# Kernel optimization log

Measured on AMD Instinct MI355X. Metric: run time of the kernel, lower is better.

The kernel has to match this reference:

```python
import jax, jax.numpy as jnp
import numpy as np

B, T, D = 64, 1024, 512
H, O = 512, 128
HALF = D // 2
ALPHA_M = 0.8


def setup_inputs() -> dict:
    key = jax.random.key(0)
    ks = jax.random.split(key, 6)
    s_in = 1.0 / np.sqrt(HALF)
    s_h = 1.0 / np.sqrt(H)
    return {
        "x": jax.random.normal(ks[0], (B, T, D), dtype=jnp.float32),
        "w1": jax.random.uniform(ks[1], (H, HALF), jnp.float32, -s_in, s_in),
        "b1": jnp.zeros((H,), jnp.float32),
        "tau1": jnp.full((H,), 3.0, jnp.float32),
        "w2": jax.random.uniform(ks[2], (H, HALF), jnp.float32, -s_in, s_in),
        "b2": jnp.zeros((H,), jnp.float32),
        "tau2": jnp.full((H,), 0.5, jnp.float32),
        "wo": jax.random.uniform(ks[3], (O, H), jnp.float32, -s_h, s_h),
        "bo": jnp.zeros((O,), jnp.float32),
    }


def reference(x, w1, b1, tau1, w2, b2, tau2, wo, bo):
    # Hoist the per-timestep branch Linears into two batched GEMMs.
    d1_in = jnp.einsum("bti,hi->tbh", x[:, :, :HALF], w1) + b1  # [T,B,H]
    d2_in = jnp.einsum("bti,hi->tbh", x[:, :, HALF:], w2) + b2  # [T,B,H]

    a1 = jax.nn.sigmoid(tau1)  # [H]
    a2 = jax.nn.sigmoid(tau2)  # [H]

    def step(carry, ins):
        d1, d2, mem = carry
        i1, i2 = ins
        d1 = a1 * d1 + (1.0 - a1) * i1
        d2 = a2 * d2 + (1.0 - a2) * i2
        mem = ALPHA_M * mem + (1.0 - ALPHA_M) * (d1 + d2)
        return (d1, d2, mem), mem

    z = jnp.zeros((x.shape[0], tau1.shape[0]), x.dtype)
    _, mems = jax.lax.scan(step, (z, z, z), (d1_in, d2_in))  # mems: [T,B,H]

    # Output projection + sigmoid, vectorized over all timesteps.
    out = jax.nn.sigmoid(jnp.einsum("tbh,oh->bto", mems, wo) + bo)  # [B,T,O]
    return out
```

## Files before the change

kernel.cpp:

```cpp
#include <hip/hip_runtime.h>


#define B_    64
#define T_    1024
#define D_    512
#define H_    512
#define O_    128
#define HALF_ 256
#define CLEN  32
#define NC    32

typedef __attribute__((ext_vector_type(4))) float        f32x4;
typedef __attribute__((ext_vector_type(2))) float        f32x2;
typedef __attribute__((ext_vector_type(8))) short        s16x8;
typedef __attribute__((ext_vector_type(4))) unsigned int u32x4;

__device__ __forceinline__ unsigned short f2bf(float f) {
    unsigned u = __float_as_uint(f);
    return (unsigned short)((u + 0x7fffu + ((u >> 16) & 1u)) >> 16);
}
__device__ __forceinline__ unsigned packbf(float a, float b) {
    return (unsigned)f2bf(a) | ((unsigned)f2bf(b) << 16);
}
__device__ __forceinline__ float bflo(unsigned u) { return __uint_as_float(u << 16); }
__device__ __forceinline__ float bfhi(unsigned u) { return __uint_as_float(u & 0xffff0000u); }
__device__ __forceinline__ float sigf(float x) { return 1.f / (1.f + __expf(-x)); }
__device__ __forceinline__ float guard(float dn) {
    if (fabsf(dn) < 1e-6f) dn = (dn < 0.f ? -1e-6f : 1e-6f);
    return dn;
}
__device__ __forceinline__ float pw32(float a) {
    float t = a * a; t *= t; t *= t; t *= t; t *= t; return t;
}

typedef const __attribute__((address_space(1))) unsigned int gu32;
typedef __attribute__((address_space(3))) unsigned int      lu32;
__device__ __forceinline__ void gl_lds16(const void* g, void* l) {
    __builtin_amdgcn_global_load_lds((gu32*)g, (lu32*)l, 16, 0, 0);
}

__global__ __launch_bounds__(256) void gtab_kernel(
    const float* __restrict__ tau1, const float* __restrict__ tau2,
    float* __restrict__ G1, float* __restrict__ G2)
{
    const int h = blockIdx.x * 256 + threadIdx.x;
    const float a1 = sigf(tau1[h]), a2 = sigf(tau2[h]);
    const float c1 = 0.2f * a1 / guard(0.8f - a1);
    const float c2 = 0.2f * a2 / guard(0.8f - a2);
    float pm = 1.f, p1 = 1.f, p2 = 1.f;
    for (int k = 0; k < CLEN; ++k) {
        pm *= 0.8f; p1 *= a1; p2 *= a2;
        G1[k * H_ + h] = c1 * (pm - p1);
        G2[k * H_ + h] = c2 * (pm - p2);
    }
}

__global__ __launch_bounds__(256) void cast_kernel(const float* __restrict__ x,
                                                   unsigned int* __restrict__ xb) {
    size_t i = ((size_t)blockIdx.x * 256 + threadIdx.x) * 8;
    f32x4 a = *(const f32x4*)(x + i);
    f32x4 b = *(const f32x4*)(x + i + 4);
    u32x4 p;
    p.x = packbf(a.x, a.y); p.y = packbf(a.z, a.w);
    p.z = packbf(b.x, b.y); p.w = packbf(b.z, b.w);
    *(u32x4*)(xb + i / 2) = p;
}

__global__ __launch_bounds__(256, 2) void gemm1f_kernel(
    const unsigned short* __restrict__ xb, const float* __restrict__ w1,
    const float* __restrict__ w2,
    const float* __restrict__ b1, const float* __restrict__ tau1,
    const float* __restrict__ b2, const float* __restrict__ tau2,
    unsigned int* __restrict__ mems,
    float* __restrict__ Sd1, float* __restrict__ Sd2, float* __restrict__ Sm)
{
    __shared__ short smem[32768];
    short* As  = smem;
    short* Bs  = smem + 8192;
    short* d1L = smem + 16384;
    short* d2L = smem;

    const int nt = blockIdx.x;
    const int mt = blockIdx.y;
    const int b  = mt >> 3;
    const int t0 = (mt & 7) << 7;

    const int tid = threadIdx.x, l = tid & 63, wv = tid >> 6;
    const int ln = l & 15, qd = l >> 4;
    const int wm = (wv & 1) << 6, wn = (wv >> 1) << 6;

    for (int br = 0; br < 2; ++br) {
        const float* w = br ? w2 : w1;
        const unsigned short* abase = xb + (size_t)(mt * 128) * D_ + br * HALF_;
        const float* wbase = w + (size_t)(nt * 128) * HALF_;

        f32x4 acc[4][4] = {};

        for (int kt = 0; kt < HALF_; kt += 64) {
            #pragma unroll
            for (int i = 0; i < 4; ++i) {
                int ch = wv * 4 + i;
                int r  = ch * 8 + (l >> 3);
                int kbl = (l & 7) ^ (r & 7);
                gl_lds16(abase + (size_t)r * D_ + kt + kbl * 8, &As[ch * 512 + l * 8]);
            }
            #pragma unroll
            for (int i = 0; i < 4; ++i) {
                int gi = i * 256 + tid;
                int r = gi >> 3, kbp = gi & 7, kbl = kbp ^ (r & 7);
                const float* src = wbase + (size_t)r * HALF_ + kt + kbl * 8;
                f32x4 b0 = *(const f32x4*)src;
                f32x4 b1v = *(const f32x4*)(src + 4);
                u32x4 pb;
                pb.x = packbf(b0.x, b0.y); pb.y = packbf(b0.z, b0.w);
                pb.z = packbf(b1v.x, b1v.y); pb.w = packbf(b1v.z, b1v.w);
                *(u32x4*)&Bs[r * 64 + kbp * 8] = pb;
            }
            __syncthreads();
            #pragma unroll
            for (int ks = 0; ks < 64; ks += 32) {
                s16x8 af[4], bfv[4];
                #pragma unroll
                for (int i = 0; i < 4; ++i) {
                    int r = wm + i * 16 + ln;
                    int kbp = ((ks >> 3) + qd) ^ (r & 7);
                    af[i] = *(const s16x8*)&As[r * 64 + kbp * 8];
                }
                #pragma unroll
                for (int j = 0; j < 4; ++j) {
                    int r = wn + j * 16 + ln;
                    int kbp = ((ks >> 3) + qd) ^ (r & 7);
                    bfv[j] = *(const s16x8*)&Bs[r * 64 + kbp * 8];
                }
                #pragma unroll
                for (int i = 0; i < 4; ++i)
                    #pragma unroll
                    for (int j = 0; j < 4; ++j)
                        acc[i][j] = __builtin_amdgcn_mfma_f32_16x16x32_bf16(
                            af[i], bfv[j], acc[i][j], 0, 0, 0);
            }
            __syncthreads();
        }

        short* dL = br ? d2L : d1L;
        #pragma unroll
        for (int i = 0; i < 4; ++i)
            #pragma unroll
            for (int j = 0; j < 4; ++j)
                #pragma unroll
                for (int r = 0; r < 4; ++r)
                    dL[(wm + i * 16 + qd * 4 + r) * 128 + wn + j * 16 + ln] =
                        (short)f2bf(acc[i][j][r]);
    }
    __syncthreads();

    const int cl  = tid >> 6;
    const int h2l = tid & 63;
    const int hl0 = h2l << 1;
    const int hg0 = nt * 128 + hl0;
    const int cg  = ((mt & 7) << 2) + cl;

    const float a1a = sigf(tau1[hg0]), a1b = sigf(tau1[hg0 + 1]);
    const float a2a = sigf(tau2[hg0]), a2b = sigf(tau2[hg0 + 1]);
    const float o1a = 1.f - a1a, o1b = 1.f - a1b;
    const float o2a = 1.f - a2a, o2b = 1.f - a2b;
    const float bb1a = b1[hg0], bb1b = b1[hg0 + 1];
    const float bb2a = b2[hg0], bb2b = b2[hg0 + 1];

    float d1a = 0.f, d1b = 0.f, d2a = 0.f, d2b = 0.f, ma = 0.f, mb = 0.f;
    const size_t mrow = (size_t)(b * T_ + t0 + cl * CLEN) * (H_ / 2) + nt * 64 + h2l;

    #pragma unroll 8
    for (int k = 0; k < CLEN; ++k) {
        unsigned u1 = *(const unsigned*)&d1L[(cl * CLEN + k) * 128 + hl0];
        unsigned u2 = *(const unsigned*)&d2L[(cl * CLEN + k) * 128 + hl0];
        float i1a = bflo(u1) + bb1a, i1b = bfhi(u1) + bb1b;
        float i2a = bflo(u2) + bb2a, i2b = bfhi(u2) + bb2b;
        d1a = a1a * d1a + o1a * i1a;  d1b = a1b * d1b + o1b * i1b;
        d2a = a2a * d2a + o2a * i2a;  d2b = a2b * d2b + o2b * i2b;
        ma = 0.8f * ma + 0.2f * (d1a + d2a);
        mb = 0.8f * mb + 0.2f * (d1b + d2b);
        mems[mrow + (size_t)k * (H_ / 2)] = packbf(ma, mb);
    }

    const size_t si = (size_t)(cg * B_ + b) * H_ + hg0;
    f32x2 v;
    v.x = d1a; v.y = d1b; *(f32x2*)&Sd1[si] = v;
    v.x = d2a; v.y = d2b; *(f32x2*)&Sd2[si] = v;
    v.x = ma;  v.y = mb;  *(f32x2*)&Sm[si]  = v;
}

__global__ __launch_bounds__(128) void scanB_kernel(
    const float* __restrict__ Sd1, const float* __restrict__ Sd2,
    const float* __restrict__ Sm,
    const float* __restrict__ tau1, const float* __restrict__ tau2,
    float* __restrict__ D1, float* __restrict__ D2, float* __restrict__ DM)
{
    const int g = blockIdx.x * 128 + threadIdx.x;
    const int h2 = g & 255, b = g >> 8, h0 = h2 << 1;

    const float a1a = sigf(tau1[h0]), a1b = sigf(tau1[h0 + 1]);
    const float a2a = sigf(tau2[h0]), a2b = sigf(tau2[h0 + 1]);
    const float amL = pw32(0.8f);
    const float a1La = pw32(a1a), a1Lb = pw32(a1b);
    const float a2La = pw32(a2a), a2Lb = pw32(a2b);

    const float c1a = 0.2f * a1a / guard(0.8f - a1a);
    const float c1b = 0.2f * a1b / guard(0.8f - a1b);
    const float c2a = 0.2f * a2a / guard(0.8f - a2a);
    const float c2b = 0.2f * a2b / guard(0.8f - a2b);

    const float g1La = c1a * (amL - a1La), g1Lb = c1b * (amL - a1Lb);
    const float g2La = c2a * (amL - a2La), g2Lb = c2b * (amL - a2Lb);

    float D1a = 0.f, D1b = 0.f, D2a = 0.f, D2b = 0.f, Ma = 0.f, Mb = 0.f;
    for (int c = 0; c < NC; ++c) {
        const size_t si = (size_t)(c * B_ + b) * H_ + h0;
        f32x2 v;
        v.x = D1a; v.y = D1b; *(f32x2*)&D1[si] = v;
        v.x = D2a; v.y = D2b; *(f32x2*)&D2[si] = v;
        v.x = Ma;  v.y = Mb;  *(f32x2*)&DM[si] = v;
        f32x2 s1 = *(const f32x2*)&Sd1[si];
        f32x2 s2 = *(const f32x2*)&Sd2[si];
        f32x2 sm = *(const f32x2*)&Sm[si];
        float nMa = amL * Ma + D1a * g1La + D2a * g2La + sm.x;
        float nMb = amL * Mb + D1b * g1Lb + D2b * g2Lb + sm.y;
        D1a = a1La * D1a + s1.x;  D1b = a1Lb * D1b + s1.y;
        D2a = a2La * D2a + s2.x;  D2b = a2Lb * D2b + s2.y;
        Ma = nMa;  Mb = nMb;
    }
}

__global__ __launch_bounds__(256, 2) void gemm2f_kernel(
    const unsigned short* __restrict__ mems, const float* __restrict__ wo,
    const float* __restrict__ bo,
    const float* __restrict__ G1, const float* __restrict__ G2,
    const float* __restrict__ D1, const float* __restrict__ D2,
    const float* __restrict__ DM, float* __restrict__ out)
{
    __shared__ short As[128 * 64];
    __shared__ short Bs[128 * 64];
    __shared__ float PMl[CLEN];

    const int mt = blockIdx.x;
    const int b = mt >> 3, c0 = (mt & 7) << 2;
    const int tid = threadIdx.x, l = tid & 63, wv = tid >> 6;
    const int ln = l & 15, qd = l >> 4;
    const int wm = (wv & 1) << 6, wn = (wv >> 1) << 6;

    if (tid < CLEN) {
        float pm = 1.f;
        for (int k = 0; k <= tid; ++k) pm *= 0.8f;
        PMl[tid] = pm;
    }
    __syncthreads();

    f32x4 acc[4][4] = {};
    const unsigned short* abase = mems + (size_t)(mt * 128) * H_;

    for (int kt = 0; kt < H_; kt += 64) {
        #pragma unroll
        for (int i = 0; i < 4; ++i) {
            int gi = i * 256 + tid;
            int r = gi >> 3, kbp = gi & 7, kbl = kbp ^ (r & 7);
            int h0 = kt + kbl * 8;
            int k = r & 31, c = c0 + (r >> 5);
            size_t dbase = (size_t)(c * B_ + b) * H_ + h0;
            f32x4 d1a = *(const f32x4*)&D1[dbase], d1b = *(const f32x4*)&D1[dbase + 4];
            f32x4 d2a = *(const f32x4*)&D2[dbase], d2b = *(const f32x4*)&D2[dbase + 4];
            f32x4 dma = *(const f32x4*)&DM[dbase], dmb = *(const f32x4*)&DM[dbase + 4];
            f32x4 g1a = *(const f32x4*)&G1[k * H_ + h0], g1b = *(const f32x4*)&G1[k * H_ + h0 + 4];
            f32x4 g2a = *(const f32x4*)&G2[k * H_ + h0], g2b = *(const f32x4*)&G2[k * H_ + h0 + 4];
            float pm = PMl[k];
            u32x4 mv = *(const u32x4*)(abase + (size_t)r * H_ + h0);
            float v0 = bflo(mv.x) + d1a.x * g1a.x + d2a.x * g2a.x + dma.x * pm;
            float v1 = bfhi(mv.x) + d1a.y * g1a.y + d2a.y * g2a.y + dma.y * pm;
            float v2 = bflo(mv.y) + d1a.z * g1a.z + d2a.z * g2a.z + dma.z * pm;
            float v3 = bfhi(mv.y) + d1a.w * g1a.w + d2a.w * g2a.w + dma.w * pm;
            float v4 = bflo(mv.z) + d1b.x * g1b.x + d2b.x * g2b.x + dmb.x * pm;
            float v5 = bfhi(mv.z) + d1b.y * g1b.y + d2b.y * g2b.y + dmb.y * pm;
            float v6 = bflo(mv.w) + d1b.z * g1b.z + d2b.z * g2b.z + dmb.z * pm;
            float v7 = bfhi(mv.w) + d1b.w * g1b.w + d2b.w * g2b.w + dmb.w * pm;
            u32x4 p;
            p.x = packbf(v0, v1); p.y = packbf(v2, v3);
            p.z = packbf(v4, v5); p.w = packbf(v6, v7);
            *(u32x4*)&As[r * 64 + kbp * 8] = p;
        }
        #pragma unroll
        for (int i = 0; i < 4; ++i) {
            int gi = i * 256 + tid;
            int r = gi >> 3, kbp = gi & 7, kbl = kbp ^ (r & 7);
            const float* src = wo + (size_t)r * H_ + kt + kbl * 8;
            f32x4 b0 = *(const f32x4*)src;
            f32x4 b1v = *(const f32x4*)(src + 4);
            u32x4 pb;
            pb.x = packbf(b0.x, b0.y); pb.y = packbf(b0.z, b0.w);
            pb.z = packbf(b1v.x, b1v.y); pb.w = packbf(b1v.z, b1v.w);
            *(u32x4*)&Bs[r * 64 + kbp * 8] = pb;
        }
        __syncthreads();
        #pragma unroll
        for (int ks = 0; ks < 64; ks += 32) {
            s16x8 af[4], bfv[4];
            #pragma unroll
            for (int i = 0; i < 4; ++i) {
                int r = wm + i * 16 + ln;
                int kbp = ((ks >> 3) + qd) ^ (r & 7);
                af[i] = *(const s16x8*)&As[r * 64 + kbp * 8];
            }
            #pragma unroll
            for (int j = 0; j < 4; ++j) {
                int r = wn + j * 16 + ln;
                int kbp = ((ks >> 3) + qd) ^ (r & 7);
                bfv[j] = *(const s16x8*)&Bs[r * 64 + kbp * 8];
            }
            #pragma unroll
            for (int i = 0; i < 4; ++i)
                #pragma unroll
                for (int j = 0; j < 4; ++j)
                    acc[i][j] = __builtin_amdgcn_mfma_f32_16x16x32_bf16(
                        af[i], bfv[j], acc[i][j], 0, 0, 0);
        }
        __syncthreads();
    }

    float bov[4];
    #pragma unroll
    for (int j = 0; j < 4; ++j) bov[j] = bo[wn + j * 16 + ln];

    float* orow = out + (size_t)(mt * 128 + wm + qd * 4) * O_ + wn + ln;
    #pragma unroll
    for (int i = 0; i < 4; ++i)
        #pragma unroll
        for (int j = 0; j < 4; ++j)
            #pragma unroll
            for (int r = 0; r < 4; ++r) {
                float v = acc[i][j][r] + bov[j];
                orow[(size_t)(i * 16 + r) * O_ + j * 16] = 1.f / (1.f + __expf(-v));
            }
}

extern "C" void kernel_launch(void* const* d_in, const int* in_sizes, int n_in,
                              void* d_out, int out_size, void* d_ws, size_t ws_size,
                              hipStream_t stream) {
    const float* x    = (const float*)d_in[0];
    const float* w1   = (const float*)d_in[1];
    const float* b1   = (const float*)d_in[2];
    const float* tau1 = (const float*)d_in[3];
    const float* w2   = (const float*)d_in[4];
    const float* b2   = (const float*)d_in[5];
    const float* tau2 = (const float*)d_in[6];
    const float* wo   = (const float*)d_in[7];
    const float* bo   = (const float*)d_in[8];
    float* out = (float*)d_out;

    char* w = (char*)d_ws;
    unsigned short* xb   = (unsigned short*)(w);
    unsigned int*   mems = (unsigned int*)(w + (size_t)64 * 1024 * 1024);
    float* Sd1 = (float*)(w + (size_t)128 * 1024 * 1024);
    float* Sd2 = Sd1 + (1u << 20);
    float* Sm  = Sd1 + (2u << 20);
    float* D1  = Sd1 + (3u << 20);
    float* D2  = Sd1 + (4u << 20);
    float* DM  = Sd1 + (5u << 20);
    float* G1  = Sd1 + (6u << 20);
    float* G2  = G1 + CLEN * H_;

    gtab_kernel<<<dim3(2), 256, 0, stream>>>(tau1, tau2, G1, G2);
    cast_kernel<<<dim3(16384), 256, 0, stream>>>(x, (unsigned int*)xb);
    gemm1f_kernel<<<dim3(4, 512), 256, 0, stream>>>(xb, w1, w2, b1, tau1, b2, tau2,
                                                    mems, Sd1, Sd2, Sm);
    scanB_kernel<<<dim3(128), 128, 0, stream>>>(Sd1, Sd2, Sm, tau1, tau2, D1, D2, DM);
    gemm2f_kernel<<<dim3(512), 256, 0, stream>>>((const unsigned short*)mems, wo, bo,
                                                 G1, G2, D1, D2, DM, out);
}
```

Baseline: 364.8 us.

## Fuse x bf16 cast into gemm1, precast weights, halve scan chunk length

Removes the separate cast of x to bf16, which wrote and reread a 64 MB intermediate. gemm1 now reads fp32 x directly and converts it to bf16 while staging. The weights are precast once to bf16 by a small kernel so the GEMMs can load them asynchronously straight into LDS. gemm1 is restructured so each block owns 64 rows and loops over all four H tiles, so x is read once per block; it uses smaller tiles and targets higher occupancy. The chunk length drops to 16, giving 64 chunks, which shortens the serial scan per chunk but doubles the carry state that scanB has to combine.

```diff
diff --git a/kernel.cpp b/kernel.cpp
--- a/kernel.cpp
+++ b/kernel.cpp
@@ -7,8 +7,8 @@
 #define H_    512
 #define O_    128
 #define HALF_ 256
-#define CLEN  32
-#define NC    32
+#define CLEN  16
+#define NC    64
 
 typedef __attribute__((ext_vector_type(4))) float        f32x4;
 typedef __attribute__((ext_vector_type(2))) float        f32x2;
@@ -29,14 +29,32 @@
     if (fabsf(dn) < 1e-6f) dn = (dn < 0.f ? -1e-6f : 1e-6f);
     return dn;
 }
-__device__ __forceinline__ float pw32(float a) {
-    float t = a * a; t *= t; t *= t; t *= t; t *= t; return t;
+__device__ __forceinline__ float pw16(float a) {
+    float t = a * a; t *= t; t *= t; t *= t; return t;
 }
 
 typedef const __attribute__((address_space(1))) unsigned int gu32;
 typedef __attribute__((address_space(3))) unsigned int      lu32;
 __device__ __forceinline__ void gl_lds16(const void* g, void* l) {
     __builtin_amdgcn_global_load_lds((gu32*)g, (lu32*)l, 16, 0, 0);
+}
+
+__global__ __launch_bounds__(256) void wcast_kernel(
+    const float* __restrict__ w1, const float* __restrict__ w2,
+    const float* __restrict__ wo, unsigned int* __restrict__ dst)
+{
+    int g = blockIdx.x * 256 + threadIdx.x;
+    int i = g * 8;
+    const float* src; int off;
+    if (i < 131072)      { src = w1; off = i; }
+    else if (i < 262144) { src = w2; off = i - 131072; }
+    else                 { src = wo; off = i - 262144; }
+    f32x4 a = *(const f32x4*)(src + off);
+    f32x4 b = *(const f32x4*)(src + off + 4);
+    u32x4 p;
+    p.x = packbf(a.x, a.y); p.y = packbf(a.z, a.w);
+    p.z = packbf(b.x, b.y); p.w = packbf(b.z, b.w);
+    *(u32x4*)(dst + i / 2) = p;
 }
 
 __global__ __launch_bounds__(256) void gtab_kernel(
@@ -55,139 +73,138 @@
     }
 }
 
-__global__ __launch_bounds__(256) void cast_kernel(const float* __restrict__ x,
-                                                   unsigned int* __restrict__ xb) {
-    size_t i = ((size_t)blockIdx.x * 256 + threadIdx.x) * 8;
-    f32x4 a = *(const f32x4*)(x + i);
-    f32x4 b = *(const f32x4*)(x + i + 4);
-    u32x4 p;
-    p.x = packbf(a.x, a.y); p.y = packbf(a.z, a.w);
-    p.z = packbf(b.x, b.y); p.w = packbf(b.z, b.w);
-    *(u32x4*)(xb + i / 2) = p;
-}
-
-__global__ __launch_bounds__(256, 2) void gemm1f_kernel(
-    const unsigned short* __restrict__ xb, const float* __restrict__ w1,
-    const float* __restrict__ w2,
+__global__ __launch_bounds__(256, 4) void gemm1f_kernel(
+    const float* __restrict__ x,
+    const unsigned short* __restrict__ w1b, const unsigned short* __restrict__ w2b,
     const float* __restrict__ b1, const float* __restrict__ tau1,
     const float* __restrict__ b2, const float* __restrict__ tau2,
     unsigned int* __restrict__ mems,
     float* __restrict__ Sd1, float* __restrict__ Sd2, float* __restrict__ Sm)
 {
-    __shared__ short smem[32768];
-    short* As  = smem;
-    short* Bs  = smem + 8192;
-    short* d1L = smem + 16384;
-    short* d2L = smem;
-
-    const int nt = blockIdx.x;
-    const int mt = blockIdx.y;
-    const int b  = mt >> 3;
-    const int t0 = (mt & 7) << 7;
+    __shared__ short smem[20480];
+    short* As = smem;
+    short* Bs = smem + 4096;
+
+    const int mt = blockIdx.x;
+    const int b  = mt >> 4;
+    const int tb = mt & 15;
+    const int m0 = mt * 64;
 
     const int tid = threadIdx.x, l = tid & 63, wv = tid >> 6;
     const int ln = l & 15, qd = l >> 4;
-    const int wm = (wv & 1) << 6, wn = (wv >> 1) << 6;
-
-    for (int br = 0; br < 2; ++br) {
-        const float* w = br ? w2 : w1;
-        const unsigned short* abase = xb + (size_t)(mt * 128) * D_ + br * HALF_;
-        const float* wbase = w + (size_t)(nt * 128) * HALF_;
-
-        f32x4 acc[4][4] = {};
-
-        for (int kt = 0; kt < HALF_; kt += 64) {
-            #pragma unroll
-            for (int i = 0; i < 4; ++i) {
-                int ch = wv * 4 + i;
-                int r  = ch * 8 + (l >> 3);
-                int kbl = (l & 7) ^ (r & 7);
-                gl_lds16(abase + (size_t)r * D_ + kt + kbl * 8, &As[ch * 512 + l * 8]);
+    const int wm = (wv & 1) << 5;
+    const int wn = (wv >> 1) << 6;
+
+    for (int nt = 0; nt < 4; ++nt) {
+        for (int br = 0; br < 2; ++br) {
+            const unsigned short* wbase = (br ? w2b : w1b) + (size_t)(nt * 128) * HALF_;
+            const float* ab = x + (size_t)m0 * D_ + br * HALF_;
+
+            f32x4 acc[2][4] = {};
+
+            for (int kt = 0; kt < HALF_; kt += 64) {
+                #pragma unroll
+                for (int i = 0; i < 4; ++i) {
+                    int ch = wv * 4 + i;
+                    int r  = ch * 8 + (l >> 3);
+                    int kbl = (l & 7) ^ (r & 7);
+                    gl_lds16(wbase + (size_t)r * HALF_ + kt + kbl * 8,
+                             &Bs[ch * 512 + l * 8]);
+                }
+                #pragma unroll
+                for (int i = 0; i < 2; ++i) {
+                    int gi = i * 256 + tid;
+                    int r = gi >> 3, kbp = gi & 7, kbl = kbp ^ (r & 7);
+                    const float* src = ab + (size_t)r * D_ + kt + kbl * 8;
+                    f32x4 a0 = *(const f32x4*)src;
+                    f32x4 a1v = *(const f32x4*)(src + 4);
+                    u32x4 pa;
+                    pa.x = packbf(a0.x, a0.y); pa.y = packbf(a0.z, a0.w);
+                    pa.z = packbf(a1v.x, a1v.y); pa.w = packbf(a1v.z, a1v.w);
+                    *(u32x4*)&As[r * 64 + kbp * 8] = pa;
+                }
+                __syncthreads();
+                #pragma unroll
+                for (int ks = 0; ks < 64; ks += 32) {
+                    s16x8 af[2], bfv[4];
+                    #pragma unroll
+                    for (int i = 0; i < 2; ++i) {
+                        int r = wm + i * 16 + ln;
+                        int kbp = ((ks >> 3) + qd) ^ (r & 7);
+                        af[i] = *(const s16x8*)&As[r * 64 + kbp * 8];
+                    }
+                    #pragma unroll
+                    for (int j = 0; j < 4; ++j) {
+                        int r = wn + j * 16 + ln;
+                        int kbp = ((ks >> 3) + qd) ^ (r & 7);
+                        bfv[j] = *(const s16x8*)&Bs[r * 64 + kbp * 8];
+                    }
+                    #pragma unroll
+                    for (int i = 0; i < 2; ++i)
+                        #pragma unroll
+                        for (int j = 0; j < 4; ++j)
+                            acc[i][j] = __builtin_amdgcn_mfma_f32_16x16x32_bf16(
+                                af[i], bfv[j], acc[i][j], 0, 0, 0);
+                }
+                __syncthreads();
             }
-            #pragma unroll
-            for (int i = 0; i < 4; ++i) {
-                int gi = i * 256 + tid;
-                int r = gi >> 3, kbp = gi & 7, kbl = kbp ^ (r & 7);
-                const float* src = wbase + (size_t)r * HALF_ + kt + kbl * 8;
-                f32x4 b0 = *(const f32x4*)src;
-                f32x4 b1v = *(const f32x4*)(src + 4);
-                u32x4 pb;
-                pb.x = packbf(b0.x, b0.y); pb.y = packbf(b0.z, b0.w);
-                pb.z = packbf(b1v.x, b1v.y); pb.w = packbf(b1v.z, b1v.w);
-                *(u32x4*)&Bs[r * 64 + kbp * 8] = pb;
-            }
-            __syncthreads();
-            #pragma unroll
-            for (int ks = 0; ks < 64; ks += 32) {
-                s16x8 af[4], bfv[4];
-                #pragma unroll
-                for (int i = 0; i < 4; ++i) {
-                    int r = wm + i * 16 + ln;
-                    int kbp = ((ks >> 3) + qd) ^ (r & 7);
-                    af[i] = *(const s16x8*)&As[r * 64 + kbp * 8];
-                }
-                #pragma unroll
-                for (int j = 0; j < 4; ++j) {
-                    int r = wn + j * 16 + ln;
-                    int kbp = ((ks >> 3) + qd) ^ (r & 7);
-                    bfv[j] = *(const s16x8*)&Bs[r * 64 + kbp * 8];
-                }
-                #pragma unroll
-                for (int i = 0; i < 4; ++i)
+
+            short* dS = br ? smem : (smem + 12288);
+            #pragma unroll
+            for (int i = 0; i < 2; ++i)
+                #pragma unroll
+                for (int j = 0; j < 4; ++j)
                     #pragma unroll
-                    for (int j = 0; j < 4; ++j)
-                        acc[i][j] = __builtin_amdgcn_mfma_f32_16x16x32_bf16(
-                            af[i], bfv[j], acc[i][j], 0, 0, 0);
-            }
-            __syncthreads();
-        }
-
-        short* dL = br ? d2L : d1L;
-        #pragma unroll
-        for (int i = 0; i < 4; ++i)
-            #pragma unroll
-            for (int j = 0; j < 4; ++j)
-                #pragma unroll
-                for (int r = 0; r < 4; ++r)
-                    dL[(wm + i * 16 + qd * 4 + r) * 128 + wn + j * 16 + ln] =
-                        (short)f2bf(acc[i][j][r]);
-    }
-    __syncthreads();
-
-    const int cl  = tid >> 6;
-    const int h2l = tid & 63;
-    const int hl0 = h2l << 1;
-    const int hg0 = nt * 128 + hl0;
-    const int cg  = ((mt & 7) << 2) + cl;
-
-    const float a1a = sigf(tau1[hg0]), a1b = sigf(tau1[hg0 + 1]);
-    const float a2a = sigf(tau2[hg0]), a2b = sigf(tau2[hg0 + 1]);
-    const float o1a = 1.f - a1a, o1b = 1.f - a1b;
-    const float o2a = 1.f - a2a, o2b = 1.f - a2b;
-    const float bb1a = b1[hg0], bb1b = b1[hg0 + 1];
-    const float bb2a = b2[hg0], bb2b = b2[hg0 + 1];
-
-    float d1a = 0.f, d1b = 0.f, d2a = 0.f, d2b = 0.f, ma = 0.f, mb = 0.f;
-    const size_t mrow = (size_t)(b * T_ + t0 + cl * CLEN) * (H_ / 2) + nt * 64 + h2l;
-
-    #pragma unroll 8
-    for (int k = 0; k < CLEN; ++k) {
-        unsigned u1 = *(const unsigned*)&d1L[(cl * CLEN + k) * 128 + hl0];
-        unsigned u2 = *(const unsigned*)&d2L[(cl * CLEN + k) * 128 + hl0];
-        float i1a = bflo(u1) + bb1a, i1b = bfhi(u1) + bb1b;
-        float i2a = bflo(u2) + bb2a, i2b = bfhi(u2) + bb2b;
-        d1a = a1a * d1a + o1a * i1a;  d1b = a1b * d1b + o1b * i1b;
-        d2a = a2a * d2a + o2a * i2a;  d2b = a2b * d2b + o2b * i2b;
-        ma = 0.8f * ma + 0.2f * (d1a + d2a);
-        mb = 0.8f * mb + 0.2f * (d1b + d2b);
-        mems[mrow + (size_t)k * (H_ / 2)] = packbf(ma, mb);
-    }
-
-    const size_t si = (size_t)(cg * B_ + b) * H_ + hg0;
-    f32x2 v;
-    v.x = d1a; v.y = d1b; *(f32x2*)&Sd1[si] = v;
-    v.x = d2a; v.y = d2b; *(f32x2*)&Sd2[si] = v;
-    v.x = ma;  v.y = mb;  *(f32x2*)&Sm[si]  = v;
+                    for (int r = 0; r < 4; ++r) {
+                        int t = wm + i * 16 + qd * 4 + r;
+                        int h = wn + j * 16 + ln;
+                        int word = t * 64 + ((h >> 1) ^ (qd << 3));
+                        dS[word * 2 + (h & 1)] = (short)f2bf(acc[i][j][r]);
+                    }
+        }
+        __syncthreads();
+
+        const int cl  = tid >> 6;
+        const int h2l = tid & 63;
+        const int hg0 = nt * 128 + (h2l << 1);
+        const int cg  = tb * 4 + cl;
+
+        const float a1a = sigf(tau1[hg0]), a1b = sigf(tau1[hg0 + 1]);
+        const float a2a = sigf(tau2[hg0]), a2b = sigf(tau2[hg0 + 1]);
+        const float o1a = 1.f - a1a, o1b = 1.f - a1b;
+        const float o2a = 1.f - a2a, o2b = 1.f - a2b;
+        const float bb1a = b1[hg0], bb1b = b1[hg0 + 1];
+        const float bb2a = b2[hg0], bb2b = b2[hg0 + 1];
+
+        const unsigned* d1p = (const unsigned*)(smem + 12288);
+        const unsigned* d2p = (const unsigned*)smem;
+
+        float d1a = 0.f, d1b = 0.f, d2a = 0.f, d2b = 0.f, ma = 0.f, mb = 0.f;
+        const size_t mrow = ((size_t)(b * T_ + tb * 64 + cl * CLEN)) * (H_ / 2)
+                            + nt * 64 + h2l;
+
+        #pragma unroll
+        for (int k = 0; k < CLEN; ++k) {
+            int tw = (cl * CLEN + k) * 64;
+            int sw = h2l ^ (((k >> 2) & 3) << 3);
+            unsigned u1 = d1p[tw + sw];
+            unsigned u2 = d2p[tw + sw];
+            float i1a = bflo(u1) + bb1a, i1b = bfhi(u1) + bb1b;
+            float i2a = bflo(u2) + bb2a, i2b = bfhi(u2) + bb2b;
+            d1a = a1a * d1a + o1a * i1a;  d1b = a1b * d1b + o1b * i1b;
+            d2a = a2a * d2a + o2a * i2a;  d2b = a2b * d2b + o2b * i2b;
+            ma = 0.8f * ma + 0.2f * (d1a + d2a);
+            mb = 0.8f * mb + 0.2f * (d1b + d2b);
+            mems[mrow + (size_t)k * (H_ / 2)] = packbf(ma, mb);
+        }
+
+        const size_t si = (size_t)(cg * B_ + b) * H_ + hg0;
+        f32x2 v;
+        v.x = d1a; v.y = d1b; *(f32x2*)&Sd1[si] = v;
+        v.x = d2a; v.y = d2b; *(f32x2*)&Sd2[si] = v;
+        v.x = ma;  v.y = mb;  *(f32x2*)&Sm[si]  = v;
+        __syncthreads();
+    }
 }
 
 __global__ __launch_bounds__(128) void scanB_kernel(
@@ -201,9 +218,9 @@
 
     const float a1a = sigf(tau1[h0]), a1b = sigf(tau1[h0 + 1]);
     const float a2a = sigf(tau2[h0]), a2b = sigf(tau2[h0 + 1]);
-    const float amL = pw32(0.8f);
-    const float a1La = pw32(a1a), a1Lb = pw32(a1b);
-    const float a2La = pw32(a2a), a2Lb = pw32(a2b);
+    const float amL = pw16(0.8f);
+    const float a1La = pw16(a1a), a1Lb = pw16(a1b);
+    const float a2La = pw16(a2a), a2Lb = pw16(a2b);
 
     const float c1a = 0.2f * a1a / guard(0.8f - a1a);
     const float c1b = 0.2f * a1b / guard(0.8f - a1b);
@@ -232,7 +249,7 @@
 }
 
 __global__ __launch_bounds__(256, 2) void gemm2f_kernel(
-    const unsigned short* __restrict__ mems, const float* __restrict__ wo,
+    const unsigned short* __restrict__ mems, const unsigned short* __restrict__ wob,
     const float* __restrict__ bo,
     const float* __restrict__ G1, const float* __restrict__ G2,
     const float* __restrict__ D1, const float* __restrict__ D2,
@@ -243,7 +260,7 @@
     __shared__ float PMl[CLEN];
 
     const int mt = blockIdx.x;
-    const int b = mt >> 3, c0 = (mt & 7) << 2;
+    const int b = mt >> 3, c0 = (mt & 7) << 3;
     const int tid = threadIdx.x, l = tid & 63, wv = tid >> 6;
     const int ln = l & 15, qd = l >> 4;
     const int wm = (wv & 1) << 6, wn = (wv >> 1) << 6;
@@ -261,10 +278,17 @@
     for (int kt = 0; kt < H_; kt += 64) {
         #pragma unroll
         for (int i = 0; i < 4; ++i) {
+            int ch = wv * 4 + i;
+            int r  = ch * 8 + (l >> 3);
+            int kbl = (l & 7) ^ (r & 7);
+            gl_lds16(wob + (size_t)r * H_ + kt + kbl * 8, &Bs[ch * 512 + l * 8]);
+        }
+        #pragma unroll
+        for (int i = 0; i < 4; ++i) {
             int gi = i * 256 + tid;
             int r = gi >> 3, kbp = gi & 7, kbl = kbp ^ (r & 7);
             int h0 = kt + kbl * 8;
-            int k = r & 31, c = c0 + (r >> 5);
+            int k = r & (CLEN - 1), c = c0 + (r >> 4);
             size_t dbase = (size_t)(c * B_ + b) * H_ + h0;
             f32x4 d1a = *(const f32x4*)&D1[dbase], d1b = *(const f32x4*)&D1[dbase + 4];
             f32x4 d2a = *(const f32x4*)&D2[dbase], d2b = *(const f32x4*)&D2[dbase + 4];
@@ -286,18 +310,6 @@
             p.z = packbf(v4, v5); p.w = packbf(v6, v7);
             *(u32x4*)&As[r * 64 + kbp * 8] = p;
         }
-        #pragma unroll
-        for (int i = 0; i < 4; ++i) {
-            int gi = i * 256 + tid;
-            int r = gi >> 3, kbp = gi & 7, kbl = kbp ^ (r & 7);
-            const float* src = wo + (size_t)r * H_ + kt + kbl * 8;
-            f32x4 b0 = *(const f32x4*)src;
-            f32x4 b1v = *(const f32x4*)(src + 4);
-            u32x4 pb;
-            pb.x = packbf(b0.x, b0.y); pb.y = packbf(b0.z, b0.w);
-            pb.z = packbf(b1v.x, b1v.y); pb.w = packbf(b1v.z, b1v.w);
-            *(u32x4*)&Bs[r * 64 + kbp * 8] = pb;
-        }
         __syncthreads();
         #pragma unroll
         for (int ks = 0; ks < 64; ks += 32) {
@@ -354,23 +366,26 @@
     const float* bo   = (const float*)d_in[8];
     float* out = (float*)d_out;
 
-    char* w = (char*)d_ws;
-    unsigned short* xb   = (unsigned short*)(w);
-    unsigned int*   mems = (unsigned int*)(w + (size_t)64 * 1024 * 1024);
-    float* Sd1 = (float*)(w + (size_t)128 * 1024 * 1024);
-    float* Sd2 = Sd1 + (1u << 20);
-    float* Sm  = Sd1 + (2u << 20);
-    float* D1  = Sd1 + (3u << 20);
-    float* D2  = Sd1 + (4u << 20);
-    float* DM  = Sd1 + (5u << 20);
-    float* G1  = Sd1 + (6u << 20);
+    char* wsp = (char*)d_ws;
+    unsigned int* mems = (unsigned int*)wsp;
+    float* Sd1 = (float*)(wsp + (size_t)64 * 1024 * 1024);
+    const size_t SARR = (size_t)NC * B_ * H_;
+    float* Sd2 = Sd1 + SARR;
+    float* Sm  = Sd1 + 2 * SARR;
+    float* D1  = Sd1 + 3 * SARR;
+    float* D2  = Sd1 + 4 * SARR;
+    float* DM  = Sd1 + 5 * SARR;
+    float* G1  = Sd1 + 6 * SARR;
     float* G2  = G1 + CLEN * H_;
-
+    unsigned short* w1b = (unsigned short*)(G2 + CLEN * H_);
+    unsigned short* w2b = w1b + 131072;
+    unsigned short* wob = w2b + 131072;
+
+    wcast_kernel<<<dim3(160), 256, 0, stream>>>(w1, w2, wo, (unsigned int*)w1b);
     gtab_kernel<<<dim3(2), 256, 0, stream>>>(tau1, tau2, G1, G2);
-    cast_kernel<<<dim3(16384), 256, 0, stream>>>(x, (unsigned int*)xb);
-    gemm1f_kernel<<<dim3(4, 512), 256, 0, stream>>>(xb, w1, w2, b1, tau1, b2, tau2,
-                                                    mems, Sd1, Sd2, Sm);
+    gemm1f_kernel<<<dim3(1024), 256, 0, stream>>>(x, w1b, w2b, b1, tau1, b2, tau2,
+                                                  mems, Sd1, Sd2, Sm);
     scanB_kernel<<<dim3(128), 128, 0, stream>>>(Sd1, Sd2, Sm, tau1, tau2, D1, D2, DM);
-    gemm2f_kernel<<<dim3(512), 256, 0, stream>>>((const unsigned short*)mems, wo, bo,
+    gemm2f_kernel<<<dim3(512), 256, 0, stream>>>((const unsigned short*)mems, wob, bo,
                                                  G1, G2, D1, D2, DM, out);
 }
```

Result: slower. 396.3 us (+8.7%).
